# Kernel optimization log

Measured on AMD Instinct MI355X. Metric: run time of the kernel, lower is better.

Reference implementation:

```python
import jax, jax.numpy as jnp
import numpy as np

DIM = 512
EPS = 1e-08
LN_EPS = 1e-05  # torch LayerNorm default


def layer_norm(x, g, b):
    mu = jnp.mean(x, axis=-1, keepdims=True)
    var = jnp.mean(jnp.square(x - mu), axis=-1, keepdims=True)
    return (x - mu) * jax.lax.rsqrt(var + LN_EPS) * g + b


def setup_inputs() -> dict:
    key = jax.random.key(0)
    ks = jax.random.split(key, 10)
    B, NQ, NK, D = 8, 1024, 2048, DIM
    s = 1.0 / np.sqrt(D)
    return {
        "inputs": jax.random.normal(ks[0], (B, NQ, D), jnp.float32),
        "context": jax.random.normal(ks[1], (B, NK, D), jnp.float32),
        "ln_in_g": jnp.ones((D,), jnp.float32),
        "ln_in_b": jnp.zeros((D,), jnp.float32),
        "ln_ctx_g": jnp.ones((D,), jnp.float32),
        "ln_ctx_b": jnp.zeros((D,), jnp.float32),
        "Wq": jax.random.uniform(ks[2], (D, D), jnp.float32, -s, s),
        "bq": jax.random.uniform(ks[3], (D,), jnp.float32, -s, s),
        "Wk": jax.random.uniform(ks[4], (D, D), jnp.float32, -s, s),
        "bk": jax.random.uniform(ks[5], (D,), jnp.float32, -s, s),
        "Wv": jax.random.uniform(ks[6], (D, D), jnp.float32, -s, s),
        "bv": jax.random.uniform(ks[7], (D,), jnp.float32, -s, s),
    }


def reference(inputs, context, ln_in_g, ln_in_b, ln_ctx_g, ln_ctx_b, Wq, bq, Wk, bk, Wv, bv):
    x = layer_norm(inputs, ln_in_g, ln_in_b)
    c = layer_norm(context, ln_ctx_g, ln_ctx_b)
    q = x @ Wq.T + bq  # [B, Nq, D]
    k = c @ Wk.T + bk  # [B, Nk, D]
    v = c @ Wv.T + bv  # [B, Nk, D]
    scale = DIM ** (-0.5)
    dots = jnp.einsum('bid,bjd->bij', q, k) * scale  # [B, Nq, Nk]
    attn = jax.nn.softmax(dots, axis=1) + EPS  # softmax over query axis
    attn = attn / jnp.sum(attn, axis=2, keepdims=True)  # renorm over key axis
    updates = jnp.einsum('bjd,bij->bid', v, attn)
    return updates
```

## Files before the change

### kernel.cpp

```cpp
#include <hip/hip_runtime.h>

using u16 = unsigned short;
typedef __attribute__((ext_vector_type(8))) short short8;
typedef __attribute__((ext_vector_type(4))) float floatx4;

#define NQ 1024
#define NK 2048
#define DD 512

__device__ __forceinline__ u16 f2bf(float f) {
  union { float f; unsigned u; } x; x.f = f;
  unsigned r = (x.u + 0x7fffu + ((x.u >> 16) & 1u)) >> 16;
  return (u16)r;
}
__device__ __forceinline__ float bf2f(u16 u) {
  union { unsigned u; float f; } x; x.u = ((unsigned)u) << 16; return x.f;
}
__device__ __forceinline__ float wave_sum(float v) {
#pragma unroll
  for (int off = 32; off > 0; off >>= 1) v += __shfl_down(v, off, 64);
  return v;
}
__device__ __forceinline__ void gload16(const u16* g, const u16* l) {
  __builtin_amdgcn_global_load_lds(
      (const __attribute__((address_space(1))) void*)g,
      (__attribute__((address_space(3))) void*)l, 16, 0, 0);
}

__global__ __launch_bounds__(256) void ln_prep(
    const float* __restrict__ X1, const float* __restrict__ G1,
    const float* __restrict__ B1, u16* __restrict__ Y1,
    const float* __restrict__ X2, const float* __restrict__ G2,
    const float* __restrict__ B2, u16* __restrict__ Y2,
    const float* __restrict__ Wq, const float* __restrict__ Wk,
    const float* __restrict__ Wv, u16* __restrict__ wqb,
    u16* __restrict__ wkb, u16* __restrict__ wvb, float* __restrict__ Zero) {
  int row = blockIdx.x;
  const int t = threadIdx.x;
  if (row >= 24576) {
    int bx = row - 24576;
    if (bx < 768) {
      const float* src = bx < 256 ? Wq : (bx < 512 ? Wk : Wv);
      u16* dst = bx < 256 ? wqb : (bx < 512 ? wkb : wvb);
      int i = ((bx & 255) * 256 + t) * 4;
      float4 v = *(const float4*)(src + i);
      ushort4 o;
      o.x = f2bf(v.x); o.y = f2bf(v.y); o.z = f2bf(v.z); o.w = f2bf(v.w);
      *(ushort4*)(dst + i) = o;
    } else {
      int i = ((bx - 768) * 256 + t) * 4;
      float4 z = {0.f, 0.f, 0.f, 0.f};
      *(float4*)(Zero + i) = z;
    }
    return;
  }
  const float *X, *G, *Bv; u16* Y;
  if (row < 8192) { X = X1; G = G1; Bv = B1; Y = Y1; }
  else { row -= 8192; X = X2; G = G2; Bv = B2; Y = Y2; }
  const float2 v = ((const float2*)(X + (long)row * DD))[t];
  float s = v.x + v.y, ss = v.x * v.x + v.y * v.y;
  __shared__ float red[8];
  float a = wave_sum(s), b = wave_sum(ss);
  if ((t & 63) == 0) { red[t >> 6] = a; red[4 + (t >> 6)] = b; }
  __syncthreads();
  float tot = red[0] + red[1] + red[2] + red[3];
  float tss = red[4] + red[5] + red[6] + red[7];
  float mu = tot * (1.f / DD);
  float var = tss * (1.f / DD) - mu * mu;
  float rs = rsqrtf(var + 1e-5f);
  float2 g2 = ((const float2*)G)[t];
  float2 b2 = ((const float2*)Bv)[t];
  ushort2 o;
  o.x = f2bf((v.x - mu) * rs * g2.x + b2.x);
  o.y = f2bf((v.y - mu) * rs * g2.y + b2.y);
  ((ushort2*)(Y + (long)row * DD))[t] = o;
}

__global__ __launch_bounds__(256) void gemm_proj(
    const u16* __restrict__ A1, const u16* __restrict__ W1,
    const float* __restrict__ b1, u16* __restrict__ C1,
    const u16* __restrict__ A2, const u16* __restrict__ W2,
    const float* __restrict__ b2, u16* __restrict__ C2) {
  __shared__ u16 lA[128 * 64];
  __shared__ u16 lB[128 * 64];
  const u16 *A, *B; const float* bias; u16* Cout;
  int m0 = blockIdx.x * 128;
  if (blockIdx.x < 64) { A = A1; B = W1; bias = b1; Cout = C1; }
  else { A = A2; B = W2; bias = b2; Cout = C2; m0 = (blockIdx.x - 64) * 128; }
  const int n0 = blockIdx.y * 128;
  const int t = threadIdx.x, wave = t >> 6, lane = t & 63;
  const int fm = lane & 15, fq = lane >> 4;
  const int wm = (wave >> 1) * 64, wn = (wave & 1) * 64;

  const int srow = t >> 3;
  const int swz = ((t & 7) ^ (srow & 7)) * 8;
  const u16* gA = A + (long)(m0 + srow) * 512 + swz;
  const u16* gB = B + (long)(n0 + srow) * 512 + swz;
  u16* dA = lA + wave * 512;
  u16* dB = lB + wave * 512;

  floatx4 acc[4][4];
#pragma unroll
  for (int x = 0; x < 4; ++x)
#pragma unroll
    for (int y = 0; y < 4; ++y) { floatx4 z = {0.f, 0.f, 0.f, 0.f}; acc[x][y] = z; }

#pragma unroll 1
  for (int kt = 0; kt < 8; ++kt) {
    gload16(gA, dA);
    gload16(gA + 32L * 512, dA + 2048);
    gload16(gA + 64L * 512, dA + 4096);
    gload16(gA + 96L * 512, dA + 6144);
    gload16(gB, dB);
    gload16(gB + 32L * 512, dB + 2048);
    gload16(gB + 64L * 512, dB + 4096);
    gload16(gB + 96L * 512, dB + 6144);
    gA += 64; gB += 64;
    __syncthreads();
#pragma unroll
    for (int ks = 0; ks < 2; ++ks) {
      short8 af[4], bfr[4];
      const int csl = ((ks * 4 + fq) ^ (fm & 7)) * 8;
#pragma unroll
      for (int x = 0; x < 4; ++x)
        af[x] = *(const short8*)&lA[(wm + x * 16 + fm) * 64 + csl];
#pragma unroll
      for (int y = 0; y < 4; ++y)
        bfr[y] = *(const short8*)&lB[(wn + y * 16 + fm) * 64 + csl];
#pragma unroll
      for (int x = 0; x < 4; ++x)
#pragma unroll
        for (int y = 0; y < 4; ++y)
          acc[x][y] = __builtin_amdgcn_mfma_f32_16x16x32_bf16(af[x], bfr[y], acc[x][y], 0, 0, 0);
    }
    __syncthreads();
  }

  float bs[4];
#pragma unroll
  for (int y = 0; y < 4; ++y) bs[y] = bias[n0 + wn + y * 16 + fm];
#pragma unroll
  for (int x = 0; x < 4; ++x)
#pragma unroll
    for (int y = 0; y < 4; ++y)
#pragma unroll
      for (int r = 0; r < 4; ++r) {
        int row = m0 + wm + x * 16 + fq * 4 + r;
        int col = n0 + wn + y * 16 + fm;
        Cout[(long)row * 512 + col] = f2bf(acc[x][y][r] + bs[y]);
      }
}

__global__ __launch_bounds__(256) void qk_vproj(
    const u16* __restrict__ qb, const u16* __restrict__ kb,
    u16* __restrict__ E, float* __restrict__ Z,
    const u16* __restrict__ wvb, const u16* __restrict__ cb,
    const float* __restrict__ bv, u16* __restrict__ vT,
    float* __restrict__ colV, float scale) {
  __shared__ u16 lA[128 * 64];
  __shared__ u16 lB[128 * 64];
  __shared__ float colred[128];

  const int bx = blockIdx.x;
  const bool is_qk = bx < 1024;
  const u16 *A, *B;
  int m0, n0, b;
  if (is_qk) {
    b = bx & 7;
    n0 = ((bx >> 3) & 15) * 128;
    m0 = (bx >> 7) * 128;
    A = qb + (long)b * (1024L * 512);
    B = kb + (long)b * (2048L * 512);
  } else {
    int e = bx - 1024;
    m0 = (e & 3) * 128;
    n0 = (e >> 2) * 128;
    b = 0;
    A = wvb;
    B = cb;
  }
  const int t = threadIdx.x, wave = t >> 6, lane = t & 63;
  const int fm = lane & 15, fq = lane >> 4;
  const int wm = (wave >> 1) * 64, wn = (wave & 1) * 64;

  const int srow = t >> 3;
  const int swz = ((t & 7) ^ (srow & 7)) * 8;
  const u16* gA = A + (long)(m0 + srow) * 512 + swz;
  const u16* gB = B + (long)(n0 + srow) * 512 + swz;
  u16* dA = lA + wave * 512;
  u16* dB = lB + wave * 512;

  floatx4 acc[4][4];
#pragma unroll
  for (int x = 0; x < 4; ++x)
#pragma unroll
    for (int y = 0; y < 4; ++y) { floatx4 z = {0.f, 0.f, 0.f, 0.f}; acc[x][y] = z; }

#pragma unroll 1
  for (int kt = 0; kt < 8; ++kt) {
    gload16(gA, dA);
    gload16(gA + 32L * 512, dA + 2048);
    gload16(gA + 64L * 512, dA + 4096);
    gload16(gA + 96L * 512, dA + 6144);
    gload16(gB, dB);
    gload16(gB + 32L * 512, dB + 2048);
    gload16(gB + 64L * 512, dB + 4096);
    gload16(gB + 96L * 512, dB + 6144);
    gA += 64; gB += 64;
    __syncthreads();
#pragma unroll
    for (int ks = 0; ks < 2; ++ks) {
      short8 af[4], bfr[4];
      const int csl = ((ks * 4 + fq) ^ (fm & 7)) * 8;
#pragma unroll
      for (int x = 0; x < 4; ++x)
        af[x] = *(const short8*)&lA[(wm + x * 16 + fm) * 64 + csl];
#pragma unroll
      for (int y = 0; y < 4; ++y)
        bfr[y] = *(const short8*)&lB[(wn + y * 16 + fm) * 64 + csl];
#pragma unroll
      for (int x = 0; x < 4; ++x)
#pragma unroll
        for (int y = 0; y < 4; ++y)
          acc[x][y] = __builtin_amdgcn_mfma_f32_16x16x32_bf16(af[x], bfr[y], acc[x][y], 0, 0, 0);
    }
    __syncthreads();
  }

  if (is_qk) {
    float s4[4] = {0.f, 0.f, 0.f, 0.f};
    u16* Eg = E + (long)b * (1024L * 2048);
#pragma unroll
    for (int x = 0; x < 4; ++x)
#pragma unroll
      for (int y = 0; y < 4; ++y)
#pragma unroll
        for (int r = 0; r < 4; ++r) {
          int row = m0 + wm + x * 16 + fq * 4 + r;
          int col = n0 + wn + y * 16 + fm;
          float e = __expf(acc[x][y][r] * scale);
          s4[y] += e;
          Eg[(long)row * 2048 + col] = f2bf(e);
        }
#pragma unroll
    for (int y = 0; y < 4; ++y) {
      s4[y] += __shfl_xor(s4[y], 16, 64);
      s4[y] += __shfl_xor(s4[y], 32, 64);
    }
    if (t < 128) colred[t] = 0.f;
    __syncthreads();
    if (fq == 0) {
#pragma unroll
      for (int y = 0; y < 4; ++y) atomicAdd(&colred[wn + y * 16 + fm], s4[y]);
    }
    __syncthreads();
    if (t < 128) atomicAdd(&Z[b * 2048 + n0 + t], colred[t]);
  } else {
    const int bb = n0 >> 11;
    const int j0c = n0 & 2047;
    float bsr[4][4];
#pragma unroll
    for (int x = 0; x < 4; ++x)
#pragma unroll
      for (int r = 0; r < 4; ++r)
        bsr[x][r] = bv[m0 + wm + x * 16 + fq * 4 + r];
    u16* Cg = vT + (long)bb * (512L * 2048) + j0c;
    float rs[4][4];
#pragma unroll
    for (int x = 0; x < 4; ++x)
#pragma unroll
      for (int r = 0; r < 4; ++r) rs[x][r] = 0.f;
#pragma unroll
    for (int x = 0; x < 4; ++x)
#pragma unroll
      for (int y = 0; y < 4; ++y)
#pragma unroll
        for (int r = 0; r < 4; ++r) {
          int rowd = m0 + wm + x * 16 + fq * 4 + r;
          int col = wn + y * 16 + fm;
          float val = acc[x][y][r] + bsr[x][r];
          rs[x][r] += val;
          Cg[(long)rowd * 2048 + col] = f2bf(val);
        }
#pragma unroll
    for (int x = 0; x < 4; ++x)
#pragma unroll
      for (int r = 0; r < 4; ++r) {
        float s = rs[x][r];
        s += __shfl_xor(s, 1, 64);
        s += __shfl_xor(s, 2, 64);
        s += __shfl_xor(s, 4, 64);
        s += __shfl_xor(s, 8, 64);
        if (fm == 0)
          atomicAdd(&colV[bb * 512 + m0 + wm + x * 16 + fq * 4 + r], s);
      }
  }
}

__global__ __launch_bounds__(256) void scaleV(u16* __restrict__ vT,
                                              const float* __restrict__ Z) {
  const long f = ((long)blockIdx.x * 256 + threadIdx.x) * 8;
  const int b = (int)(f >> 20);
  const int j = (int)(f & 2047);
  const float* zp = Z + b * 2048 + j;
  short8 v = *(const short8*)(vT + f);
  short8 o;
#pragma unroll
  for (int k = 0; k < 8; ++k)
    o[k] = (short)f2bf(bf2f((u16)v[k]) * __builtin_amdgcn_rcpf(zp[k]));
  *(short8*)(vT + f) = o;
}

__global__ __launch_bounds__(256) void gemm_pv(const u16* __restrict__ E,
    const u16* __restrict__ V, const float* __restrict__ colV,
    const float* __restrict__ Z, float* __restrict__ out) {
  __shared__ u16 lA[64 * 64];
  __shared__ u16 lB[64 * 64];
  __shared__ u16 sZb[2048];
  const int id = blockIdx.x;
  const int b = id & 7;
  const int m0 = ((id >> 3) & 15) * 64, n0 = (id >> 7) * 64;
  const int t = threadIdx.x, wave = t >> 6, lane = t & 63;
  const int fm = lane & 15, fq = lane >> 4;
  const int wm = (wave >> 1) * 32, wn = (wave & 1) * 32;

  {
    int i = t * 8;
    float4 z0 = *(const float4*)(Z + b * 2048 + i);
    float4 z1 = *(const float4*)(Z + b * 2048 + i + 4);
    short8 o;
    o[0] = (short)f2bf(__builtin_amdgcn_rcpf(z0.x));
    o[1] = (short)f2bf(__builtin_amdgcn_rcpf(z0.y));
    o[2] = (short)f2bf(__builtin_amdgcn_rcpf(z0.z));
    o[3] = (short)f2bf(__builtin_amdgcn_rcpf(z0.w));
    o[4] = (short)f2bf(__builtin_amdgcn_rcpf(z1.x));
    o[5] = (short)f2bf(__builtin_amdgcn_rcpf(z1.y));
    o[6] = (short)f2bf(__builtin_amdgcn_rcpf(z1.z));
    o[7] = (short)f2bf(__builtin_amdgcn_rcpf(z1.w));
    *(short8*)&sZb[i] = o;
  }

  const int srow = t >> 3;
  const int swz = ((t & 7) ^ (srow & 7)) * 8;
  const u16* gA = E + (long)b * (1024L * 2048) + (long)(m0 + srow) * 2048 + swz;
  const u16* gB = V + (long)b * (512L * 2048) + (long)(n0 + srow) * 2048 + swz;
  u16* dA = lA + wave * 512;
  u16* dB = lB + wave * 512;

  floatx4 acc[2][2];
  floatx4 accR[2];
#pragma unroll
  for (int x = 0; x < 2; ++x) {
    floatx4 z = {0.f, 0.f, 0.f, 0.f};
    accR[x] = z;
#pragma unroll
    for (int y = 0; y < 2; ++y) acc[x][y] = z;
  }

#pragma unroll 1
  for (int kt = 0; kt < 32; ++kt) {
    gload16(gA, dA);
    gload16(gA + 32L * 2048, dA + 2048);
    gload16(gB, dB);
    gload16(gB + 32L * 2048, dB + 2048);
    gA += 64; gB += 64;
    __syncthreads();
#pragma unroll
    for (int ks = 0; ks < 2; ++ks) {
      short8 af[2], bfr[2];
      const int chunk = ks * 4 + fq;
      const int csl = (chunk ^ (fm & 7)) * 8;
#pragma unroll
      for (int x = 0; x < 2; ++x)
        af[x] = *(const short8*)&lA[(wm + x * 16 + fm) * 64 + csl];
#pragma unroll
      for (int y = 0; y < 2; ++y)
        bfr[y] = *(const short8*)&lB[(wn + y * 16 + fm) * 64 + csl];
      short8 zf = *(const short8*)&sZb[kt * 64 + chunk * 8];
#pragma unroll
      for (int x = 0; x < 2; ++x) {
#pragma unroll
        for (int y = 0; y < 2; ++y)
          acc[x][y] = __builtin_amdgcn_mfma_f32_16x16x32_bf16(af[x], bfr[y], acc[x][y], 0, 0, 0);
        accR[x] = __builtin_amdgcn_mfma_f32_16x16x32_bf16(af[x], zf, accR[x], 0, 0, 0);
      }
    }
    __syncthreads();
  }

  float cv[2];
#pragma unroll
  for (int y = 0; y < 2; ++y) cv[y] = colV[b * 512 + n0 + wn + y * 16 + fm];
  float* og = out + (long)b * (1024L * 512);
#pragma unroll
  for (int x = 0; x < 2; ++x)
#pragma unroll
    for (int r = 0; r < 4; ++r) {
      float invR = __builtin_amdgcn_rcpf(accR[x][r] + 2048.f * 1e-8f);
      int row = m0 + wm + x * 16 + fq * 4 + r;
#pragma unroll
      for (int y = 0; y < 2; ++y) {
        int col = n0 + wn + y * 16 + fm;
        og[(long)row * 512 + col] = (acc[x][y][r] + 1e-8f * cv[y]) * invR;
      }
    }
}

extern "C" void kernel_launch(void* const* d_in, const int* in_sizes, int n_in,
                              void* d_out, int out_size, void* d_ws, size_t ws_size,
                              hipStream_t stream) {
  const float* inputs  = (const float*)d_in[0];
  const float* context = (const float*)d_in[1];
  const float* ln_in_g = (const float*)d_in[2];
  const float* ln_in_b = (const float*)d_in[3];
  const float* ln_ctx_g = (const float*)d_in[4];
  const float* ln_ctx_b = (const float*)d_in[5];
  const float* Wq = (const float*)d_in[6];
  const float* bq = (const float*)d_in[7];
  const float* Wk = (const float*)d_in[8];
  const float* bk = (const float*)d_in[9];
  const float* Wv = (const float*)d_in[10];
  const float* bv = (const float*)d_in[11];
  float* out = (float*)d_out;

  u16* ws = (u16*)d_ws;
  u16* xb  = ws;
  u16* qb  = xb + 8192L * 512;
  u16* cb  = qb + 8192L * 512;
  u16* wqb = cb + 16384L * 512;
  u16* wkb = wqb + 512L * 512;
  u16* wvb = wkb + 512L * 512;
  u16* kb  = wvb + 512L * 512;
  u16* vTs = kb + 16384L * 512;
  u16* E   = vTs + 8L * 512 * 2048;
  float* Z    = (float*)(E + 8L * 1024 * 2048);
  float* colV = Z + 8L * 2048;

  const float scale = 0.04419417382415922f;

  ln_prep<<<25364, 256, 0, stream>>>(inputs, ln_in_g, ln_in_b, xb,
                                     context, ln_ctx_g, ln_ctx_b, cb,
                                     Wq, Wk, Wv, wqb, wkb, wvb, Z);
  gemm_proj<<<dim3(192, 4, 1), 256, 0, stream>>>(xb, wqb, bq, qb,
                                                 cb, wkb, bk, kb);
  qk_vproj<<<1536, 256, 0, stream>>>(qb, kb, E, Z, wvb, cb, bv, vTs,
                                     colV, scale);
  scaleV<<<4096, 256, 0, stream>>>(vTs, Z);
  gemm_pv<<<1024, 256, 0, stream>>>(E, vTs, colV, Z, out);
}
```

Before: 226.4 us.

## Stage GEMM epilogues through LDS for coalesced stores; one-wave-per-row layernorm

Every GEMM epilogue (projection, QK exp, V projection, PV output) now writes its accumulator tile into swizzled shared memory, then stores it to global memory as 16-byte row-contiguous vectors. Previously each lane wrote scattered 2- or 4-byte elements. The layernorm kernel now assigns one row per wave instead of one row per block, with float4 loads and a shuffle-only reduction, which cuts the block count and removes a block barrier. The epilogues gain an extra barrier and LDS traffic that reuses the operand buffers.

New measurement: 207.4 us. 1.09x faster.

```diff
diff --git a/kernel.cpp b/kernel.cpp
--- a/kernel.cpp
+++ b/kernel.cpp
@@ -35,45 +35,54 @@
     const float* __restrict__ Wq, const float* __restrict__ Wk,
     const float* __restrict__ Wv, u16* __restrict__ wqb,
     u16* __restrict__ wkb, u16* __restrict__ wvb, float* __restrict__ Zero) {
-  int row = blockIdx.x;
+  const int bx = blockIdx.x;
   const int t = threadIdx.x;
-  if (row >= 24576) {
-    int bx = row - 24576;
-    if (bx < 768) {
-      const float* src = bx < 256 ? Wq : (bx < 512 ? Wk : Wv);
-      u16* dst = bx < 256 ? wqb : (bx < 512 ? wkb : wvb);
-      int i = ((bx & 255) * 256 + t) * 4;
+  if (bx >= 6144) {
+    int e = bx - 6144;
+    if (e < 768) {
+      const float* src = e < 256 ? Wq : (e < 512 ? Wk : Wv);
+      u16* dst = e < 256 ? wqb : (e < 512 ? wkb : wvb);
+      int i = ((e & 255) * 256 + t) * 4;
       float4 v = *(const float4*)(src + i);
       ushort4 o;
       o.x = f2bf(v.x); o.y = f2bf(v.y); o.z = f2bf(v.z); o.w = f2bf(v.w);
       *(ushort4*)(dst + i) = o;
     } else {
-      int i = ((bx - 768) * 256 + t) * 4;
+      int i = ((e - 768) * 256 + t) * 4;
       float4 z = {0.f, 0.f, 0.f, 0.f};
       *(float4*)(Zero + i) = z;
     }
     return;
   }
+  const int wave = t >> 6, lane = t & 63;
+  int row = bx * 4 + wave;
   const float *X, *G, *Bv; u16* Y;
   if (row < 8192) { X = X1; G = G1; Bv = B1; Y = Y1; }
   else { row -= 8192; X = X2; G = G2; Bv = B2; Y = Y2; }
-  const float2 v = ((const float2*)(X + (long)row * DD))[t];
-  float s = v.x + v.y, ss = v.x * v.x + v.y * v.y;
-  __shared__ float red[8];
-  float a = wave_sum(s), b = wave_sum(ss);
-  if ((t & 63) == 0) { red[t >> 6] = a; red[4 + (t >> 6)] = b; }
-  __syncthreads();
-  float tot = red[0] + red[1] + red[2] + red[3];
-  float tss = red[4] + red[5] + red[6] + red[7];
-  float mu = tot * (1.f / DD);
-  float var = tss * (1.f / DD) - mu * mu;
+  const float4* Xp = (const float4*)(X + (long)row * DD);
+  float4 v0 = Xp[lane * 2], v1 = Xp[lane * 2 + 1];
+  float s = v0.x + v0.y + v0.z + v0.w + v1.x + v1.y + v1.z + v1.w;
+  float ss = v0.x * v0.x + v0.y * v0.y + v0.z * v0.z + v0.w * v0.w +
+             v1.x * v1.x + v1.y * v1.y + v1.z * v1.z + v1.w * v1.w;
+  s = wave_sum(s);  s = __shfl(s, 0, 64);
+  ss = wave_sum(ss); ss = __shfl(ss, 0, 64);
+  float mu = s * (1.f / DD);
+  float var = ss * (1.f / DD) - mu * mu;
   float rs = rsqrtf(var + 1e-5f);
-  float2 g2 = ((const float2*)G)[t];
-  float2 b2 = ((const float2*)Bv)[t];
-  ushort2 o;
-  o.x = f2bf((v.x - mu) * rs * g2.x + b2.x);
-  o.y = f2bf((v.y - mu) * rs * g2.y + b2.y);
-  ((ushort2*)(Y + (long)row * DD))[t] = o;
+  const float4* Gp = (const float4*)G;
+  const float4* Bp = (const float4*)Bv;
+  float4 g0 = Gp[lane * 2], g1 = Gp[lane * 2 + 1];
+  float4 b0 = Bp[lane * 2], b1 = Bp[lane * 2 + 1];
+  short8 o;
+  o[0] = (short)f2bf((v0.x - mu) * rs * g0.x + b0.x);
+  o[1] = (short)f2bf((v0.y - mu) * rs * g0.y + b0.y);
+  o[2] = (short)f2bf((v0.z - mu) * rs * g0.z + b0.z);
+  o[3] = (short)f2bf((v0.w - mu) * rs * g0.w + b0.w);
+  o[4] = (short)f2bf((v1.x - mu) * rs * g1.x + b1.x);
+  o[5] = (short)f2bf((v1.y - mu) * rs * g1.y + b1.y);
+  o[6] = (short)f2bf((v1.z - mu) * rs * g1.z + b1.z);
+  o[7] = (short)f2bf((v1.w - mu) * rs * g1.w + b1.w);
+  *(short8*)(Y + (long)row * DD + lane * 8) = o;
 }
 
 __global__ __launch_bounds__(256) void gemm_proj(
@@ -81,8 +90,9 @@
     const float* __restrict__ b1, u16* __restrict__ C1,
     const u16* __restrict__ A2, const u16* __restrict__ W2,
     const float* __restrict__ b2, u16* __restrict__ C2) {
-  __shared__ u16 lA[128 * 64];
-  __shared__ u16 lB[128 * 64];
+  __shared__ u16 smem[16384];
+  u16* lA = smem;
+  u16* lB = smem + 8192;
   const u16 *A, *B; const float* bias; u16* Cout;
   int m0 = blockIdx.x * 128;
   if (blockIdx.x < 64) { A = A1; B = W1; bias = b1; Cout = C1; }
@@ -142,13 +152,23 @@
 #pragma unroll
   for (int x = 0; x < 4; ++x)
 #pragma unroll
-    for (int y = 0; y < 4; ++y)
+    for (int y = 0; y < 4; ++y) {
+      const int cblk = (wn >> 4) + y;
 #pragma unroll
       for (int r = 0; r < 4; ++r) {
-        int row = m0 + wm + x * 16 + fq * 4 + r;
-        int col = n0 + wn + y * 16 + fm;
-        Cout[(long)row * 512 + col] = f2bf(acc[x][y][r] + bs[y]);
+        int rowl = wm + x * 16 + fq * 4 + r;
+        smem[rowl * 128 + ((cblk ^ fq) * 16) + fm] = f2bf(acc[x][y][r] + bs[y]);
       }
+    }
+  __syncthreads();
+#pragma unroll
+  for (int p = 0; p < 8; ++p) {
+    int rowl = p * 16 + (t >> 4);
+    int c = t & 15;
+    int q = (rowl >> 2) & 3;
+    short8 v = *(const short8*)&smem[rowl * 128 + (((c >> 1) ^ q) * 16) + (c & 1) * 8];
+    *(short8*)(Cout + (long)(m0 + rowl) * 512 + n0 + c * 8) = v;
+  }
 }
 
 __global__ __launch_bounds__(256) void qk_vproj(
@@ -157,9 +177,10 @@
     const u16* __restrict__ wvb, const u16* __restrict__ cb,
     const float* __restrict__ bv, u16* __restrict__ vT,
     float* __restrict__ colV, float scale) {
-  __shared__ u16 lA[128 * 64];
-  __shared__ u16 lB[128 * 64];
+  __shared__ u16 smem[16384];
   __shared__ float colred[128];
+  u16* lA = smem;
+  u16* lB = smem + 8192;
 
   const int bx = blockIdx.x;
   const bool is_qk = bx < 1024;
@@ -229,19 +250,19 @@
 
   if (is_qk) {
     float s4[4] = {0.f, 0.f, 0.f, 0.f};
-    u16* Eg = E + (long)b * (1024L * 2048);
 #pragma unroll
     for (int x = 0; x < 4; ++x)
 #pragma unroll
-      for (int y = 0; y < 4; ++y)
+      for (int y = 0; y < 4; ++y) {
+        const int cblk = (wn >> 4) + y;
 #pragma unroll
         for (int r = 0; r < 4; ++r) {
-          int row = m0 + wm + x * 16 + fq * 4 + r;
-          int col = n0 + wn + y * 16 + fm;
+          int rowl = wm + x * 16 + fq * 4 + r;
           float e = __expf(acc[x][y][r] * scale);
           s4[y] += e;
-          Eg[(long)row * 2048 + col] = f2bf(e);
+          smem[rowl * 128 + ((cblk ^ fq) * 16) + fm] = f2bf(e);
         }
+      }
 #pragma unroll
     for (int y = 0; y < 4; ++y) {
       s4[y] += __shfl_xor(s4[y], 16, 64);
@@ -249,6 +270,15 @@
     }
     if (t < 128) colred[t] = 0.f;
     __syncthreads();
+    u16* Eg = E + (long)b * (1024L * 2048);
+#pragma unroll
+    for (int p = 0; p < 8; ++p) {
+      int rowl = p * 16 + (t >> 4);
+      int c = t & 15;
+      int q = (rowl >> 2) & 3;
+      short8 v = *(const short8*)&smem[rowl * 128 + (((c >> 1) ^ q) * 16) + (c & 1) * 8];
+      *(short8*)(Eg + (long)(m0 + rowl) * 2048 + n0 + c * 8) = v;
+    }
     if (fq == 0) {
 #pragma unroll
       for (int y = 0; y < 4; ++y) atomicAdd(&colred[wn + y * 16 + fm], s4[y]);
@@ -264,7 +294,6 @@
 #pragma unroll
       for (int r = 0; r < 4; ++r)
         bsr[x][r] = bv[m0 + wm + x * 16 + fq * 4 + r];
-    u16* Cg = vT + (long)bb * (512L * 2048) + j0c;
     float rs[4][4];
 #pragma unroll
     for (int x = 0; x < 4; ++x)
@@ -273,15 +302,26 @@
 #pragma unroll
     for (int x = 0; x < 4; ++x)
 #pragma unroll
-      for (int y = 0; y < 4; ++y)
+      for (int y = 0; y < 4; ++y) {
+        const int cblk = (wn >> 4) + y;
 #pragma unroll
         for (int r = 0; r < 4; ++r) {
-          int rowd = m0 + wm + x * 16 + fq * 4 + r;
-          int col = wn + y * 16 + fm;
+          int rowl = wm + x * 16 + fq * 4 + r;
           float val = acc[x][y][r] + bsr[x][r];
           rs[x][r] += val;
-          Cg[(long)rowd * 2048 + col] = f2bf(val);
+          smem[rowl * 128 + ((cblk ^ fq) * 16) + fm] = f2bf(val);
         }
+      }
+    __syncthreads();
+    u16* Cg = vT + (long)bb * (512L * 2048) + j0c;
+#pragma unroll
+    for (int p = 0; p < 8; ++p) {
+      int rowl = p * 16 + (t >> 4);
+      int c = t & 15;
+      int q = (rowl >> 2) & 3;
+      short8 v = *(const short8*)&smem[rowl * 128 + (((c >> 1) ^ q) * 16) + (c & 1) * 8];
+      *(short8*)(Cg + (long)(m0 + rowl) * 2048 + c * 8) = v;
+    }
 #pragma unroll
     for (int x = 0; x < 4; ++x)
 #pragma unroll
@@ -301,8 +341,7 @@
                                               const float* __restrict__ Z) {
   const long f = ((long)blockIdx.x * 256 + threadIdx.x) * 8;
   const int b = (int)(f >> 20);
-  const int j = (int)(f & 2047);
-  const float* zp = Z + b * 2048 + j;
+  const float* zp = Z + b * 2048 + (int)(f & 2047);
   short8 v = *(const short8*)(vT + f);
   short8 o;
 #pragma unroll
@@ -314,9 +353,10 @@
 __global__ __launch_bounds__(256) void gemm_pv(const u16* __restrict__ E,
     const u16* __restrict__ V, const float* __restrict__ colV,
     const float* __restrict__ Z, float* __restrict__ out) {
-  __shared__ u16 lA[64 * 64];
-  __shared__ u16 lB[64 * 64];
+  __shared__ u16 smem[8192];
   __shared__ u16 sZb[2048];
+  u16* lA = smem;
+  u16* lB = smem + 4096;
   const int id = blockIdx.x;
   const int b = id & 7;
   const int m0 = ((id >> 3) & 15) * 64, n0 = (id >> 7) * 64;
@@ -391,19 +431,30 @@
   float cv[2];
 #pragma unroll
   for (int y = 0; y < 2; ++y) cv[y] = colV[b * 512 + n0 + wn + y * 16 + fm];
-  float* og = out + (long)b * (1024L * 512);
+  float* sO = (float*)smem;
 #pragma unroll
   for (int x = 0; x < 2; ++x)
 #pragma unroll
     for (int r = 0; r < 4; ++r) {
       float invR = __builtin_amdgcn_rcpf(accR[x][r] + 2048.f * 1e-8f);
-      int row = m0 + wm + x * 16 + fq * 4 + r;
+      int rowl = wm + x * 16 + fq * 4 + r;
 #pragma unroll
       for (int y = 0; y < 2; ++y) {
-        int col = n0 + wn + y * 16 + fm;
-        og[(long)row * 512 + col] = (acc[x][y][r] + 1e-8f * cv[y]) * invR;
+        const int cblk = (wn >> 4) + y;
+        sO[rowl * 64 + ((cblk ^ fq) * 16) + fm] =
+            (acc[x][y][r] + 1e-8f * cv[y]) * invR;
       }
     }
+  __syncthreads();
+  float* og = out + (long)b * (1024L * 512);
+#pragma unroll
+  for (int p = 0; p < 4; ++p) {
+    int rowl = p * 16 + (t >> 4);
+    int c = t & 15;
+    int q = (rowl >> 2) & 3;
+    float4 v = *(const float4*)&sO[rowl * 64 + (((c >> 2) ^ q) * 16) + (c & 3) * 4];
+    *(float4*)(og + (long)(m0 + rowl) * 512 + n0 + c * 4) = v;
+  }
 }
 
 extern "C" void kernel_launch(void* const* d_in, const int* in_sizes, int n_in,
@@ -438,9 +489,9 @@
 
   const float scale = 0.04419417382415922f;
 
-  ln_prep<<<25364, 256, 0, stream>>>(inputs, ln_in_g, ln_in_b, xb,
-                                     context, ln_ctx_g, ln_ctx_b, cb,
-                                     Wq, Wk, Wv, wqb, wkb, wvb, Z);
+  ln_prep<<<6932, 256, 0, stream>>>(inputs, ln_in_g, ln_in_b, xb,
+                                    context, ln_ctx_g, ln_ctx_b, cb,
+                                    Wq, Wk, Wv, wqb, wkb, wvb, Z);
   gemm_proj<<<dim3(192, 4, 1), 256, 0, stream>>>(xb, wqb, bq, qb,
                                                  cb, wkb, bk, kb);
   qk_vproj<<<1536, 256, 0, stream>>>(qb, kb, E, Z, wvb, cb, bv, vTs,
```
